# Performance work log

Hardware: AMD Instinct MI355X
Metric: run time of the kernel (lower is better)

Reference implementation:

```python
import jax, jax.numpy as jnp
import numpy as np

N_NODES = 50000
N_EDGES = 800000
IN_CH = 128
HID_CH = 128
OUT_CH = 10
NUM_GRAPHS = 128


def setup_inputs() -> dict:
    key = jax.random.key(0)
    ks = jax.random.split(key, 10)
    x = jax.random.normal(ks[0], (N_NODES, IN_CH), dtype=jnp.float32)
    edge_index = jax.random.randint(ks[1], (2, N_EDGES), 0, N_NODES, dtype=jnp.int64)
    batch = jnp.sort(jax.random.randint(ks[2], (N_NODES,), 0, NUM_GRAPHS, dtype=jnp.int64))
    s1 = 1.0 / np.sqrt(IN_CH)
    s2 = 1.0 / np.sqrt(HID_CH)
    W1 = jax.random.uniform(ks[3], (IN_CH, HID_CH), jnp.float32, -s1, s1)
    b1 = jnp.zeros((HID_CH,), jnp.float32)
    W2 = jax.random.uniform(ks[4], (HID_CH, HID_CH), jnp.float32, -s2, s2)
    b2 = jnp.zeros((HID_CH,), jnp.float32)
    Wc = jax.random.uniform(ks[5], (HID_CH, OUT_CH), jnp.float32, -s2, s2)
    bc = jax.random.uniform(ks[6], (OUT_CH,), jnp.float32, -s2, s2)
    return {"x": x, "edge_index": edge_index, "batch": batch,
            "W1": W1, "b1": b1, "W2": W2, "b2": b2, "Wc": Wc, "bc": bc}


def _gcn_norm(edge_index, num_nodes):
    # add self-loops, compute symmetric normalization deg^-1/2[src]*deg^-1/2[dst]
    loop = jnp.arange(num_nodes, dtype=edge_index.dtype)
    src = jnp.concatenate([edge_index[0], loop])
    dst = jnp.concatenate([edge_index[1], loop])
    deg = jax.ops.segment_sum(jnp.ones_like(dst, dtype=jnp.float32), dst,
                              num_segments=num_nodes)
    dinv = jnp.where(deg > 0, jax.lax.rsqrt(deg), 0.0)
    norm = dinv[src] * dinv[dst]
    return src, dst, norm


def _gcn_conv(h, src, dst, norm, W, b, num_nodes):
    h = h @ W                                    # [N, out]
    msg = h[src] * norm[:, None]                 # [E+N, out] gather + scale
    agg = jax.ops.segment_sum(msg, dst, num_segments=num_nodes)
    return agg + b


def reference(x, edge_index, batch, W1, b1, W2, b2, Wc, bc):
    n = x.shape[0]
    src, dst, norm = _gcn_norm(edge_index, n)
    h = jax.nn.relu(_gcn_conv(x, src, dst, norm, W1, b1, n))
    h = jax.nn.relu(_gcn_conv(h, src, dst, norm, W2, b2, n))
    # global mean pool over graphs
    sums = jax.ops.segment_sum(h, batch, num_segments=NUM_GRAPHS)
    cnts = jax.ops.segment_sum(jnp.ones((n,), jnp.float32), batch,
                               num_segments=NUM_GRAPHS)
    pooled = sums / jnp.maximum(cnts, 1.0)[:, None]
    # dropout is identity in eval mode
    return pooled @ Wc + bc
```

## Files before the change

### kernel.cpp

```cpp
#include <hip/hip_runtime.h>

#define N_NODES 50000
#define N_EDGES 800000
#define CH 128
#define NOUT 10
#define NUM_GRAPHS 128
#define POOL_CHUNK 50
#define GR 64
#define GEMM_BLOCKS ((N_NODES + GR - 1) / GR)
#define FILL_SEGS 128
#define FILL_CHUNK (N_EDGES / FILL_SEGS)
#define DST_RANGE (N_NODES / 8)
#define DEG_CAP 64

typedef __attribute__((ext_vector_type(8))) short bf16x8;
typedef __attribute__((ext_vector_type(4))) float f32x4;

union FragU { uint4 u; bf16x8 s; };

__device__ __forceinline__ unsigned pack_bf16(float a, float b) {
    unsigned ua = __float_as_uint(a), ub = __float_as_uint(b);
    ua += 0x7fffu + ((ua >> 16) & 1u);
    ub += 0x7fffu + ((ub >> 16) & 1u);
    return (ua >> 16) | (ub & 0xffff0000u);
}

__device__ __forceinline__ unsigned short cvt_bf16(float v) {
    unsigned u = __float_as_uint(v);
    u += 0x7fffu + ((u >> 16) & 1u);
    return (unsigned short)(u >> 16);
}

__global__ __launch_bounds__(256) void k_prep(const float* __restrict__ W1,
                                              const float* __restrict__ W2,
                                              unsigned short* __restrict__ Wb1,
                                              unsigned short* __restrict__ Wb2,
                                              int* __restrict__ fill_pos,
                                              float* __restrict__ psum) {
    if (blockIdx.x < 2) {
        const float* W = blockIdx.x ? W2 : W1;
        unsigned short* Wb = blockIdx.x ? Wb2 : Wb1;
        for (int i = threadIdx.x; i < CH * CH; i += 256) {
            int k = i >> 7, n = i & 127;
            Wb[((((k >> 3) << 7) + n) << 3) + (k & 7)] = cvt_bf16(W[i]);
        }
    } else if (blockIdx.x < 198) {
        int idx = (blockIdx.x - 2) * 256 + threadIdx.x;
        if (idx < N_NODES) fill_pos[idx] = 0;
    } else {
        psum[(blockIdx.x - 198) * 256 + threadIdx.x] = 0.f;
    }
}

template <bool SCALE>
__device__ __forceinline__ void gemm_body9(const float* __restrict__ X,
                                           const unsigned short* __restrict__ Wb,
                                           unsigned short* __restrict__ Yb,
                                           const int* __restrict__ cnt,
                                           int bid) {
    const int tid = threadIdx.x;
    const int w = tid >> 6;
    const int lane = tid & 63;
    const int m = lane & 15;
    const int quad = lane >> 4;
    const int row0 = bid * GR + w * 16;

    int row_a = row0 + m;
    if (row_a > N_NODES - 1) row_a = N_NODES - 1;
    const float4* Xr = (const float4*)(X + (size_t)row_a * CH) + quad * 2;

    f32x4 acc[8];
    #pragma unroll
    for (int ct = 0; ct < 8; ++ct) acc[ct] = (f32x4){0.f, 0.f, 0.f, 0.f};

    const uint4* Wq = (const uint4*)Wb;
    #pragma unroll
    for (int ks = 0; ks < 4; ++ks) {
        float4 a0 = Xr[ks * 8];
        float4 a1 = Xr[ks * 8 + 1];
        FragU af;
        af.u.x = pack_bf16(a0.x, a0.y);
        af.u.y = pack_bf16(a0.z, a0.w);
        af.u.z = pack_bf16(a1.x, a1.y);
        af.u.w = pack_bf16(a1.z, a1.w);
        const int kg = ks * 4 + quad;
        #pragma unroll
        for (int ct = 0; ct < 8; ++ct) {
            FragU bfu;
            bfu.u = Wq[kg * 128 + ct * 16 + m];
            acc[ct] = __builtin_amdgcn_mfma_f32_16x16x32_bf16(af.s, bfu.s, acc[ct], 0, 0, 0);
        }
    }

    #pragma unroll
    for (int r = 0; r < 4; ++r) {
        int row = row0 + quad * 4 + r;
        if (row < N_NODES) {
            float dv = SCALE ? rsqrtf((float)(cnt[row] + 1)) : 1.0f;
            unsigned short* yrow = Yb + (size_t)row * CH + m;
            #pragma unroll
            for (int ct = 0; ct < 8; ++ct)
                yrow[ct * 16] = cvt_bf16(SCALE ? acc[ct][r] * dv : acc[ct][r]);
        }
    }
}

__global__ __launch_bounds__(256) void k_gemm_fill(const float* __restrict__ X,
                                                   const unsigned short* __restrict__ Wb,
                                                   unsigned short* __restrict__ Yb,
                                                   const int* __restrict__ src,
                                                   const int* __restrict__ dst,
                                                   int* __restrict__ fill_pos,
                                                   int* __restrict__ csr_src) {
    if (blockIdx.x < GEMM_BLOCKS) {
        gemm_body9<false>(X, Wb, Yb, nullptr, blockIdx.x);
    } else {
        const int b = blockIdx.x - GEMM_BLOCKS;
        const int rng = b & 7;
        const int seg = b >> 3;
        const int lo = rng * DST_RANGE, hi = lo + DST_RANGE;
        const int base = seg * FILL_CHUNK;
        for (int it = 0; it < FILL_CHUNK; it += 256) {
            int e = base + it + threadIdx.x;
            if (it + (int)threadIdx.x < FILL_CHUNK) {
                int d = dst[e];
                if (d >= lo && d < hi) {
                    int slot = atomicAdd(&fill_pos[d], 1);
                    if (slot < DEG_CAP) csr_src[(d << 6) + slot] = src[e];
                }
            }
        }
    }
}

__global__ __launch_bounds__(256) void k_gemm9b(const float* __restrict__ X,
                                                const unsigned short* __restrict__ Wb,
                                                unsigned short* __restrict__ Yb,
                                                const int* __restrict__ cnt) {
    gemm_body9<true>(X, Wb, Yb, cnt, blockIdx.x);
}

__global__ __launch_bounds__(256) void k_scale(unsigned* __restrict__ tb32,
                                               const int* __restrict__ cnt) {
    const int wid = blockIdx.x * 4 + (threadIdx.x >> 6);
    const int lane = threadIdx.x & 63;
    for (int r = wid; r < N_NODES; r += 1024) {
        float dv = rsqrtf((float)(cnt[r] + 1));
        unsigned u = tb32[(size_t)r * 64 + lane];
        float lo_f = __uint_as_float(u << 16) * dv;
        float hi_f = __uint_as_float(u & 0xffff0000u) * dv;
        tb32[(size_t)r * 64 + lane] = pack_bf16(lo_f, hi_f);
    }
}

__global__ __launch_bounds__(256) void k_gather_bf(const unsigned* __restrict__ tb,
                                                   const int* __restrict__ csr_src,
                                                   const int* __restrict__ cnt,
                                                   const float* __restrict__ b,
                                                   float* __restrict__ h) {
    const int wid = threadIdx.x >> 6;
    const int lane = threadIdx.x & 63;
    const int v = blockIdx.x * 4 + wid;

    int len = cnt[v];
    const float dv = rsqrtf((float)(len + 1));
    if (len > DEG_CAP) len = DEG_CAP;

    float x0 = 0.f, y0 = 0.f, x1 = 0.f, y1 = 0.f;
    float x2 = 0.f, y2 = 0.f, x3 = 0.f, y3 = 0.f;

    int u_l = 0;
    if (lane < len) u_l = csr_src[(v << 6) + lane];
    int j = 0;
    for (; j + 3 < len; j += 4) {
        int u0 = __shfl(u_l, j),     u1 = __shfl(u_l, j + 1);
        int u2 = __shfl(u_l, j + 2), u3 = __shfl(u_l, j + 3);
        unsigned r0 = tb[(size_t)u0 * 64 + lane];
        unsigned r1 = tb[(size_t)u1 * 64 + lane];
        unsigned r2 = tb[(size_t)u2 * 64 + lane];
        unsigned r3 = tb[(size_t)u3 * 64 + lane];
        x0 += __uint_as_float(r0 << 16); y0 += __uint_as_float(r0 & 0xffff0000u);
        x1 += __uint_as_float(r1 << 16); y1 += __uint_as_float(r1 & 0xffff0000u);
        x2 += __uint_as_float(r2 << 16); y2 += __uint_as_float(r2 & 0xffff0000u);
        x3 += __uint_as_float(r3 << 16); y3 += __uint_as_float(r3 & 0xffff0000u);
    }
    for (; j < len; ++j) {
        int u = __shfl(u_l, j);
        unsigned r = tb[(size_t)u * 64 + lane];
        x0 += __uint_as_float(r << 16); y0 += __uint_as_float(r & 0xffff0000u);
    }

    unsigned rs = tb[(size_t)v * 64 + lane];
    float sx = x0 + x1 + x2 + x3 + __uint_as_float(rs << 16);
    float sy = y0 + y1 + y2 + y3 + __uint_as_float(rs & 0xffff0000u);
    float2 bb = ((const float2*)b)[lane];
    float2 o;
    o.x = fmaxf(fmaf(dv, sx, bb.x), 0.f);
    o.y = fmaxf(fmaf(dv, sy, bb.y), 0.f);
    ((float2*)h)[(size_t)v * 64 + lane] = o;
}

__global__ __launch_bounds__(128) void k_pool2(const float* __restrict__ h,
                                               const int* __restrict__ batch,
                                               float* __restrict__ psum) {
    const int c = threadIdx.x;
    const int v0 = blockIdx.x * POOL_CHUNK;
    __shared__ int bg[POOL_CHUNK];
    if (c < POOL_CHUNK) bg[c] = batch[v0 + c];
    __syncthreads();

    float acc = 0.f;
    int g = bg[0];
    #pragma unroll 5
    for (int j = 0; j < POOL_CHUNK; ++j) {
        int bgj = bg[j];
        float val = h[(size_t)(v0 + j) * CH + c];
        if (bgj != g) {
            atomicAdd(&psum[g * CH + c], acc);
            acc = 0.f;
            g = bgj;
        }
        acc += val;
    }
    atomicAdd(&psum[g * CH + c], acc);
}

__global__ __launch_bounds__(128) void k_classify(const float* __restrict__ psum,
                                                  const int* __restrict__ batch,
                                                  const float* __restrict__ Wc,
                                                  const float* __restrict__ bc,
                                                  float* __restrict__ out) {
    __shared__ float p[CH];
    __shared__ float sinv;
    int g = blockIdx.x;
    int tid = threadIdx.x;
    if (tid == 0) {
        int lo = 0, hi = N_NODES;
        while (lo < hi) { int mid = (lo + hi) >> 1; if (batch[mid] < g) lo = mid + 1; else hi = mid; }
        int start = lo;
        lo = 0; hi = N_NODES;
        while (lo < hi) { int mid = (lo + hi) >> 1; if (batch[mid] < g + 1) lo = mid + 1; else hi = mid; }
        sinv = 1.0f / fmaxf((float)(lo - start), 1.0f);
    }
    __syncthreads();
    p[tid] = psum[g * CH + tid] * sinv;
    __syncthreads();
    if (tid < NOUT) {
        float acc = bc[tid];
        #pragma unroll 4
        for (int k = 0; k < CH; ++k) acc += p[k] * Wc[k * NOUT + tid];
        out[g * NOUT + tid] = acc;
    }
}

extern "C" void kernel_launch(void* const* d_in, const int* in_sizes, int n_in,
                              void* d_out, int out_size, void* d_ws, size_t ws_size,
                              hipStream_t stream) {
    const float* x     = (const float*)d_in[0];
    const int*   ei    = (const int*)d_in[1];
    const int*   batch = (const int*)d_in[2];
    const float* W1    = (const float*)d_in[3];
    const float* b1    = (const float*)d_in[4];
    const float* W2    = (const float*)d_in[5];
    const float* b2    = (const float*)d_in[6];
    const float* Wc    = (const float*)d_in[7];
    const float* bc    = (const float*)d_in[8];
    float* out = (float*)d_out;

    const int* src = ei;
    const int* dst = ei + N_EDGES;

    int*            fill_pos = (int*)d_ws;
    int*            csr_src  = fill_pos + N_NODES;
    unsigned short* wb1      = (unsigned short*)(csr_src + (size_t)N_NODES * DEG_CAP);
    unsigned short* wb2      = wb1 + CH * CH;
    unsigned short* tb       = wb2 + CH * CH;
    float*          hbuf     = (float*)(tb + (size_t)N_NODES * CH);
    float*          psum     = hbuf + (size_t)N_NODES * CH;

    k_prep<<<198 + 64, 256, 0, stream>>>(W1, W2, wb1, wb2, fill_pos, psum);

    k_gemm_fill<<<GEMM_BLOCKS + FILL_SEGS * 8, 256, 0, stream>>>(
        x, wb1, tb, src, dst, fill_pos, csr_src);

    k_scale<<<256, 256, 0, stream>>>((unsigned*)tb, fill_pos);

    k_gather_bf<<<N_NODES / 4, 256, 0, stream>>>((unsigned*)tb, csr_src, fill_pos, b1, hbuf);

    k_gemm9b<<<GEMM_BLOCKS, 256, 0, stream>>>(hbuf, wb2, tb, fill_pos);
    k_gather_bf<<<N_NODES / 4, 256, 0, stream>>>((unsigned*)tb, csr_src, fill_pos, b2, hbuf);

    k_pool2<<<N_NODES / POOL_CHUNK, 128, 0, stream>>>(hbuf, batch, psum);
    k_classify<<<NUM_GRAPHS, 128, 0, stream>>>(psum, batch, Wc, bc, out);
}
```

Baseline: 276.8 us.

## Fuse layer-1 aggregation with layer-2 GEMM and layer-2 aggregation with pooling

The layer-1 neighbor gather now writes its rows into shared memory and the layer-2 bf16 MFMA GEMM runs directly from there, so the fp32 hidden buffer no longer round-trips through global memory. The layer-2 gather is fused with mean-pool accumulation, doing per-graph atomic adds instead of writing h and reading it back. The gather inner loop is unrolled to 8 outstanding loads. Each wave now handles 16 nodes in sequence, which lowers parallelism and latency hiding compared with one node per wave across many blocks.

```diff
diff --git a/kernel.cpp b/kernel.cpp
--- a/kernel.cpp
+++ b/kernel.cpp
@@ -5,13 +5,13 @@
 #define CH 128
 #define NOUT 10
 #define NUM_GRAPHS 128
-#define POOL_CHUNK 50
 #define GR 64
 #define GEMM_BLOCKS ((N_NODES + GR - 1) / GR)
 #define FILL_SEGS 128
 #define FILL_CHUNK (N_EDGES / FILL_SEGS)
 #define DST_RANGE (N_NODES / 8)
 #define DEG_CAP 64
+#define HSTR 132
 
 typedef __attribute__((ext_vector_type(8))) short bf16x8;
 typedef __attribute__((ext_vector_type(4))) float f32x4;
@@ -52,12 +52,9 @@
     }
 }
 
-template <bool SCALE>
-__device__ __forceinline__ void gemm_body9(const float* __restrict__ X,
-                                           const unsigned short* __restrict__ Wb,
-                                           unsigned short* __restrict__ Yb,
-                                           const int* __restrict__ cnt,
-                                           int bid) {
+__device__ __forceinline__ void gemm_glb(const float* __restrict__ X,
+                                         const unsigned short* __restrict__ Wb,
+                                         unsigned short* __restrict__ Yb, int bid) {
     const int tid = threadIdx.x;
     const int w = tid >> 6;
     const int lane = tid & 63;
@@ -96,11 +93,10 @@
     for (int r = 0; r < 4; ++r) {
         int row = row0 + quad * 4 + r;
         if (row < N_NODES) {
-            float dv = SCALE ? rsqrtf((float)(cnt[row] + 1)) : 1.0f;
             unsigned short* yrow = Yb + (size_t)row * CH + m;
             #pragma unroll
             for (int ct = 0; ct < 8; ++ct)
-                yrow[ct * 16] = cvt_bf16(SCALE ? acc[ct][r] * dv : acc[ct][r]);
+                yrow[ct * 16] = cvt_bf16(acc[ct][r]);
         }
     }
 }
@@ -113,7 +109,7 @@
                                                    int* __restrict__ fill_pos,
                                                    int* __restrict__ csr_src) {
     if (blockIdx.x < GEMM_BLOCKS) {
-        gemm_body9<false>(X, Wb, Yb, nullptr, blockIdx.x);
+        gemm_glb(X, Wb, Yb, blockIdx.x);
     } else {
         const int b = blockIdx.x - GEMM_BLOCKS;
         const int rng = b & 7;
@@ -133,13 +129,6 @@
     }
 }
 
-__global__ __launch_bounds__(256) void k_gemm9b(const float* __restrict__ X,
-                                                const unsigned short* __restrict__ Wb,
-                                                unsigned short* __restrict__ Yb,
-                                                const int* __restrict__ cnt) {
-    gemm_body9<true>(X, Wb, Yb, cnt, blockIdx.x);
-}
-
 __global__ __launch_bounds__(256) void k_scale(unsigned* __restrict__ tb32,
                                                const int* __restrict__ cnt) {
     const int wid = blockIdx.x * 4 + (threadIdx.x >> 6);
@@ -153,36 +142,41 @@
     }
 }
 
-__global__ __launch_bounds__(256) void k_gather_bf(const unsigned* __restrict__ tb,
-                                                   const int* __restrict__ csr_src,
-                                                   const int* __restrict__ cnt,
-                                                   const float* __restrict__ b,
-                                                   float* __restrict__ h) {
-    const int wid = threadIdx.x >> 6;
-    const int lane = threadIdx.x & 63;
-    const int v = blockIdx.x * 4 + wid;
-
+__device__ __forceinline__ float2 gcn_row(const unsigned* __restrict__ tb,
+                                          const int* __restrict__ csr,
+                                          const int* __restrict__ cnt,
+                                          int v, int lane, float2 bb) {
     int len = cnt[v];
-    const float dv = rsqrtf((float)(len + 1));
+    float dv = rsqrtf((float)(len + 1));
     if (len > DEG_CAP) len = DEG_CAP;
 
     float x0 = 0.f, y0 = 0.f, x1 = 0.f, y1 = 0.f;
     float x2 = 0.f, y2 = 0.f, x3 = 0.f, y3 = 0.f;
 
     int u_l = 0;
-    if (lane < len) u_l = csr_src[(v << 6) + lane];
+    if (lane < len) u_l = csr[(v << 6) + lane];
     int j = 0;
-    for (; j + 3 < len; j += 4) {
+    for (; j + 7 < len; j += 8) {
         int u0 = __shfl(u_l, j),     u1 = __shfl(u_l, j + 1);
         int u2 = __shfl(u_l, j + 2), u3 = __shfl(u_l, j + 3);
+        int u4 = __shfl(u_l, j + 4), u5 = __shfl(u_l, j + 5);
+        int u6 = __shfl(u_l, j + 6), u7 = __shfl(u_l, j + 7);
         unsigned r0 = tb[(size_t)u0 * 64 + lane];
         unsigned r1 = tb[(size_t)u1 * 64 + lane];
         unsigned r2 = tb[(size_t)u2 * 64 + lane];
         unsigned r3 = tb[(size_t)u3 * 64 + lane];
+        unsigned r4 = tb[(size_t)u4 * 64 + lane];
+        unsigned r5 = tb[(size_t)u5 * 64 + lane];
+        unsigned r6 = tb[(size_t)u6 * 64 + lane];
+        unsigned r7 = tb[(size_t)u7 * 64 + lane];
         x0 += __uint_as_float(r0 << 16); y0 += __uint_as_float(r0 & 0xffff0000u);
         x1 += __uint_as_float(r1 << 16); y1 += __uint_as_float(r1 & 0xffff0000u);
         x2 += __uint_as_float(r2 << 16); y2 += __uint_as_float(r2 & 0xffff0000u);
         x3 += __uint_as_float(r3 << 16); y3 += __uint_as_float(r3 & 0xffff0000u);
+        x0 += __uint_as_float(r4 << 16); y0 += __uint_as_float(r4 & 0xffff0000u);
+        x1 += __uint_as_float(r5 << 16); y1 += __uint_as_float(r5 & 0xffff0000u);
+        x2 += __uint_as_float(r6 << 16); y2 += __uint_as_float(r6 & 0xffff0000u);
+        x3 += __uint_as_float(r7 << 16); y3 += __uint_as_float(r7 & 0xffff0000u);
     }
     for (; j < len; ++j) {
         int u = __shfl(u_l, j);
@@ -193,36 +187,105 @@
     unsigned rs = tb[(size_t)v * 64 + lane];
     float sx = x0 + x1 + x2 + x3 + __uint_as_float(rs << 16);
     float sy = y0 + y1 + y2 + y3 + __uint_as_float(rs & 0xffff0000u);
-    float2 bb = ((const float2*)b)[lane];
     float2 o;
     o.x = fmaxf(fmaf(dv, sx, bb.x), 0.f);
     o.y = fmaxf(fmaf(dv, sy, bb.y), 0.f);
-    ((float2*)h)[(size_t)v * 64 + lane] = o;
-}
-
-__global__ __launch_bounds__(128) void k_pool2(const float* __restrict__ h,
-                                               const int* __restrict__ batch,
-                                               float* __restrict__ psum) {
-    const int c = threadIdx.x;
-    const int v0 = blockIdx.x * POOL_CHUNK;
-    __shared__ int bg[POOL_CHUNK];
-    if (c < POOL_CHUNK) bg[c] = batch[v0 + c];
+    return o;
+}
+
+__global__ __launch_bounds__(256) void k_gather_gemm(const unsigned* __restrict__ tb,
+                                                     const int* __restrict__ csr,
+                                                     const int* __restrict__ cnt,
+                                                     const float* __restrict__ b1,
+                                                     const unsigned short* __restrict__ Wb2,
+                                                     unsigned short* __restrict__ tb2) {
+    __shared__ float hs[GR * HSTR];
+    const int w = threadIdx.x >> 6;
+    const int lane = threadIdx.x & 63;
+    const int base = blockIdx.x * GR + w * 16;
+
+    float2 bb = ((const float2*)b1)[lane];
+    #pragma unroll 2
+    for (int i = 0; i < 16; ++i) {
+        int v = base + i;
+        float2 o = make_float2(0.f, 0.f);
+        if (v < N_NODES) o = gcn_row(tb, csr, cnt, v, lane, bb);
+        *(float2*)&hs[(w * 16 + i) * HSTR + lane * 2] = o;
+    }
     __syncthreads();
 
-    float acc = 0.f;
-    int g = bg[0];
-    #pragma unroll 5
-    for (int j = 0; j < POOL_CHUNK; ++j) {
-        int bgj = bg[j];
-        float val = h[(size_t)(v0 + j) * CH + c];
-        if (bgj != g) {
-            atomicAdd(&psum[g * CH + c], acc);
-            acc = 0.f;
-            g = bgj;
-        }
-        acc += val;
-    }
-    atomicAdd(&psum[g * CH + c], acc);
+    const int m = lane & 15;
+    const int quad = lane >> 4;
+    const float* Ar = &hs[(w * 16 + m) * HSTR];
+
+    f32x4 acc[8];
+    #pragma unroll
+    for (int ct = 0; ct < 8; ++ct) acc[ct] = (f32x4){0.f, 0.f, 0.f, 0.f};
+
+    const uint4* Wq = (const uint4*)Wb2;
+    #pragma unroll
+    for (int ks = 0; ks < 4; ++ks) {
+        float4 a0 = *(const float4*)&Ar[ks * 32 + quad * 8];
+        float4 a1 = *(const float4*)&Ar[ks * 32 + quad * 8 + 4];
+        FragU af;
+        af.u.x = pack_bf16(a0.x, a0.y);
+        af.u.y = pack_bf16(a0.z, a0.w);
+        af.u.z = pack_bf16(a1.x, a1.y);
+        af.u.w = pack_bf16(a1.z, a1.w);
+        const int kg = ks * 4 + quad;
+        #pragma unroll
+        for (int ct = 0; ct < 8; ++ct) {
+            FragU bfu;
+            bfu.u = Wq[kg * 128 + ct * 16 + m];
+            acc[ct] = __builtin_amdgcn_mfma_f32_16x16x32_bf16(af.s, bfu.s, acc[ct], 0, 0, 0);
+        }
+    }
+
+    const int row0 = blockIdx.x * GR + w * 16;
+    #pragma unroll
+    for (int r = 0; r < 4; ++r) {
+        int row = row0 + quad * 4 + r;
+        if (row < N_NODES) {
+            float dv = rsqrtf((float)(cnt[row] + 1));
+            unsigned short* yrow = tb2 + (size_t)row * CH + m;
+            #pragma unroll
+            for (int ct = 0; ct < 8; ++ct)
+                yrow[ct * 16] = cvt_bf16(acc[ct][r] * dv);
+        }
+    }
+}
+
+__global__ __launch_bounds__(256) void k_gather_pool(const unsigned* __restrict__ tb2,
+                                                     const int* __restrict__ csr,
+                                                     const int* __restrict__ cnt,
+                                                     const int* __restrict__ batch,
+                                                     const float* __restrict__ b2,
+                                                     float* __restrict__ psum) {
+    const int w = threadIdx.x >> 6;
+    const int lane = threadIdx.x & 63;
+    const int base = blockIdx.x * GR + w * 16;
+    if (base >= N_NODES) return;
+
+    float2 bb = ((const float2*)b2)[lane];
+    float2 acc = make_float2(0.f, 0.f);
+    int cur_g = batch[base];
+
+    for (int i = 0; i < 16; ++i) {
+        int v = base + i;
+        if (v >= N_NODES) break;
+        int g = batch[v];
+        if (g != cur_g) {
+            atomicAdd(&psum[cur_g * CH + lane * 2], acc.x);
+            atomicAdd(&psum[cur_g * CH + lane * 2 + 1], acc.y);
+            acc = make_float2(0.f, 0.f);
+            cur_g = g;
+        }
+        float2 o = gcn_row(tb2, csr, cnt, v, lane, bb);
+        acc.x += o.x;
+        acc.y += o.y;
+    }
+    atomicAdd(&psum[cur_g * CH + lane * 2], acc.x);
+    atomicAdd(&psum[cur_g * CH + lane * 2 + 1], acc.y);
 }
 
 __global__ __launch_bounds__(128) void k_classify(const float* __restrict__ psum,
@@ -275,8 +338,8 @@
     unsigned short* wb1      = (unsigned short*)(csr_src + (size_t)N_NODES * DEG_CAP);
     unsigned short* wb2      = wb1 + CH * CH;
     unsigned short* tb       = wb2 + CH * CH;
-    float*          hbuf     = (float*)(tb + (size_t)N_NODES * CH);
-    float*          psum     = hbuf + (size_t)N_NODES * CH;
+    unsigned short* tb2      = tb + (size_t)N_NODES * CH;
+    float*          psum     = (float*)(tb2 + (size_t)N_NODES * CH);
 
     k_prep<<<198 + 64, 256, 0, stream>>>(W1, W2, wb1, wb2, fill_pos, psum);
 
@@ -285,11 +348,11 @@
 
     k_scale<<<256, 256, 0, stream>>>((unsigned*)tb, fill_pos);
 
-    k_gather_bf<<<N_NODES / 4, 256, 0, stream>>>((unsigned*)tb, csr_src, fill_pos, b1, hbuf);
-
-    k_gemm9b<<<GEMM_BLOCKS, 256, 0, stream>>>(hbuf, wb2, tb, fill_pos);
-    k_gather_bf<<<N_NODES / 4, 256, 0, stream>>>((unsigned*)tb, csr_src, fill_pos, b2, hbuf);
-
-    k_pool2<<<N_NODES / POOL_CHUNK, 128, 0, stream>>>(hbuf, batch, psum);
+    k_gather_gemm<<<GEMM_BLOCKS, 256, 0, stream>>>((unsigned*)tb, csr_src, fill_pos,
+                                                   b1, wb2, tb2);
+
+    k_gather_pool<<<GEMM_BLOCKS, 256, 0, stream>>>((unsigned*)tb2, csr_src, fill_pos,
+                                                   batch, b2, psum);
+
     k_classify<<<NUM_GRAPHS, 128, 0, stream>>>(psum, batch, Wc, bc, out);
 }
```

Result: slower. 298.7 us (+7.9%).
